# Kernel optimization log

Hardware: AMD Instinct MI355X
Metric: run time of the kernel (lower is better)

## Reference

```python
import jax, jax.numpy as jnp
import numpy as np

B, T, I, H, O = 128, 512, 256, 512, 256


def setup_inputs() -> dict:
    key = jax.random.key(0)
    ks = jax.random.split(key, 20)
    s_i = 1.0 / np.sqrt(I)
    s_h = 1.0 / np.sqrt(H)
    inp = {
        "x": jax.random.normal(ks[0], (B, T, I), dtype=jnp.float32),
        "Wix_w": jax.random.normal(ks[1], (H, I), dtype=jnp.float32) * s_i,
        "Wix_b": jax.random.normal(ks[2], (H,), dtype=jnp.float32) * s_i,
        "Wih_w": jax.random.normal(ks[3], (H, H), dtype=jnp.float32) * s_h,
        "Wih_b": jax.random.normal(ks[4], (H,), dtype=jnp.float32) * s_h,
        "bi": jnp.zeros((H,), dtype=jnp.float32),
        "Wfx_w": jax.random.normal(ks[5], (H, I), dtype=jnp.float32) * s_i,
        "Wfx_b": jax.random.normal(ks[6], (H,), dtype=jnp.float32) * s_i,
        "Wfh_w": jax.random.normal(ks[7], (H, H), dtype=jnp.float32) * s_h,
        "Wfh_b": jax.random.normal(ks[8], (H,), dtype=jnp.float32) * s_h,
        "bf": jnp.zeros((H,), dtype=jnp.float32),
        "Wgx_w": jax.random.normal(ks[9], (H, I), dtype=jnp.float32) * s_i,
        "Wgx_b": jax.random.normal(ks[10], (H,), dtype=jnp.float32) * s_i,
        "Wgh_w": jax.random.normal(ks[11], (H, H), dtype=jnp.float32) * s_h,
        "Wgh_b": jax.random.normal(ks[12], (H,), dtype=jnp.float32) * s_h,
        "bg": jnp.zeros((H,), dtype=jnp.float32),
        "Wox_w": jax.random.normal(ks[13], (H, I), dtype=jnp.float32) * s_i,
        "Wox_b": jax.random.normal(ks[14], (H,), dtype=jnp.float32) * s_i,
        "Woh_w": jax.random.normal(ks[15], (H, H), dtype=jnp.float32) * s_h,
        "Woh_b": jax.random.normal(ks[16], (H,), dtype=jnp.float32) * s_h,
        "bo": jnp.zeros((H,), dtype=jnp.float32),
        "Wph_w": jax.random.normal(ks[17], (O, H), dtype=jnp.float32) * s_h,
        "Wph_b": jax.random.normal(ks[18], (O,), dtype=jnp.float32) * s_h,
        "bp": jnp.zeros((O,), dtype=jnp.float32),
    }
    return inp


def reference(x, Wix_w, Wix_b, Wih_w, Wih_b, bi,
              Wfx_w, Wfx_b, Wfh_w, Wfh_b, bf,
              Wgx_w, Wgx_b, Wgh_w, Wgh_b, bg,
              Wox_w, Wox_b, Woh_w, Woh_b, bo,
              Wph_w, Wph_b, bp):
    batch = x.shape[0]
    h0 = jnp.zeros((batch, Wih_w.shape[0]), dtype=x.dtype)
    c0 = jnp.zeros_like(h0)

    # Precompute all input projections across time in 4 big GEMMs
    # (same math as per-step Linear calls, just batched over t).
    ix = jnp.einsum('bti,hi->bth', x, Wix_w) + Wix_b + bi
    fx = jnp.einsum('bti,hi->bth', x, Wfx_w) + Wfx_b + bf
    gx = jnp.einsum('bti,hi->bth', x, Wgx_w) + Wgx_b + bg
    ox = jnp.einsum('bti,hi->bth', x, Wox_w) + Wox_b + bo

    def step(carry, xt):
        h, c = carry
        ixt, fxt, gxt, oxt = xt
        i = jax.nn.sigmoid(ixt + h @ Wih_w.T + Wih_b)
        f = jax.nn.sigmoid(fxt + h @ Wfh_w.T + Wfh_b)
        g = jnp.tanh(gxt + h @ Wgh_w.T + Wgh_b)
        o = jax.nn.sigmoid(oxt + h @ Woh_w.T + Woh_b)
        c_new = g * i + c * f
        h_new = jnp.tanh(c_new) * o
        p = h_new @ Wph_w.T + Wph_b + bp
        y = jax.nn.softmax(p, axis=1)
        return (h_new, c_new), y

    # scan over time: [T, B, H] layout
    xs = (jnp.swapaxes(ix, 0, 1), jnp.swapaxes(fx, 0, 1),
          jnp.swapaxes(gx, 0, 1), jnp.swapaxes(ox, 0, 1))
    _, ys = jax.lax.scan(step, (h0, c0), xs)
    return jnp.swapaxes(ys, 0, 1)  # [B, T, O]
```

## Files before the change

### kernel.cpp

```cpp
#include <hip/hip_runtime.h>
#include <hip/hip_bf16.h>
#include <math.h>

#define B_  128
#define T_  512
#define I_  256
#define H_  512
#define O_  256
#define NP  2048
#define BT  65536
#define HB  65536

struct PrepArgs {
    const float* Whw[4];
    const float* Wxw[4];
    const float* Wxb[4];
    const float* Whb[4];
    const float* bg[4];
    const float* Wph_w;
    const float* Wph_b;
    const float* bp;
    float* Wt; float* Wg; float* WgT; float* WphT;
    float* xb; float* hb; float* pb;
};

#define PREP_TOTAL (1048576 + 524288 + 524288 + 131072 + 2048 + 2048 + 256)

__global__ __launch_bounds__(256) void k_prep(PrepArgs a) {
    int idx = blockIdx.x * 256 + threadIdx.x;
    if (idx >= PREP_TOTAL) return;
    int q = idx;
    if (q < 1048576) {
        int k = q >> 11, n = q & 2047;
        int g = n & 3, h = n >> 2;
        a.Wt[q] = a.Whw[g][h * H_ + k];
        return;
    }
    q -= 1048576;
    if (q < 524288) {
        int n = q >> 8, i = q & 255;
        int g = n & 3, h = n >> 2;
        a.Wg[q] = a.Wxw[g][h * I_ + i];
        return;
    }
    q -= 524288;
    if (q < 524288) {
        int i = q >> 11, n = q & 2047;
        int g = n & 3, h = n >> 2;
        a.WgT[q] = a.Wxw[g][h * I_ + i];
        return;
    }
    q -= 524288;
    if (q < 131072) {
        int h = q >> 8, o = q & 255;
        a.WphT[q] = a.Wph_w[o * H_ + h];
        return;
    }
    q -= 131072;
    if (q < 2048) {
        int g = q & 3, h = q >> 2;
        a.xb[q] = a.Wxb[g][h] + a.bg[g][h];
        return;
    }
    q -= 2048;
    if (q < 2048) {
        int g = q & 3, h = q >> 2;
        a.hb[q] = a.Whb[g][h];
        return;
    }
    q -= 2048;
    a.pb[q] = a.Wph_b[q] + a.bp[q];
}

__global__ __launch_bounds__(256) void k_transpose(const float* __restrict__ x,
                                                   float* __restrict__ xT2) {
    __shared__ float lds[32][33];
    int tid = threadIdx.x;
    int tx = tid & 31, ty = tid >> 5;
    int j0 = blockIdx.x * 32;
    int i0 = blockIdx.y * 32;
    int t  = j0 >> 7;
    int b0 = j0 & 127;
#pragma unroll
    for (int rr = 0; rr < 4; ++rr) {
        int jj = ty + rr * 8;
        lds[jj][tx] = x[((size_t)(b0 + jj) * T_ + t) * I_ + i0 + tx];
    }
    __syncthreads();
#pragma unroll
    for (int rr = 0; rr < 4; ++rr) {
        int ii = ty + rr * 8;
        xT2[(size_t)(i0 + ii) * BT + j0 + tx] = lds[tx][ii];
    }
}

__global__ __launch_bounds__(256, 1) void k_xgemm(const float* __restrict__ A,
                                                  const float* __restrict__ Bm,
                                                  const float* __restrict__ bias,
                                                  float* __restrict__ C) {
    __shared__ float As[16][128];
    __shared__ float Bs[16][128];
    int tid = threadIdx.x;
    int tx = tid & 15, ty = tid >> 4;
    int m0 = blockIdx.y * 128, j0 = blockIdx.x * 128;
    float acc[8][8];
#pragma unroll
    for (int i = 0; i < 8; ++i)
#pragma unroll
        for (int j = 0; j < 8; ++j) acc[i][j] = 0.f;

    for (int kt = 0; kt < I_; kt += 16) {
#pragma unroll
        for (int pp = 0; pp < 2; ++pp) {
            int p = tid + pp * 256;
            int row = p >> 2, kq = (p & 3) << 2;
            float4 av = *(const float4*)&A[(size_t)(m0 + row) * I_ + kt + kq];
            As[kq + 0][row] = av.x; As[kq + 1][row] = av.y;
            As[kq + 2][row] = av.z; As[kq + 3][row] = av.w;
        }
#pragma unroll
        for (int pp = 0; pp < 2; ++pp) {
            int p = tid + pp * 256;
            int krow = p >> 5, c4 = (p & 31) << 2;
            *(float4*)&Bs[krow][c4] =
                *(const float4*)&Bm[(size_t)(kt + krow) * BT + j0 + c4];
        }
        __syncthreads();
#pragma unroll
        for (int k = 0; k < 16; ++k) {
            float a[8], b[8];
            *(float4*)&a[0] = *(const float4*)&As[k][ty * 4];
            *(float4*)&a[4] = *(const float4*)&As[k][64 + ty * 4];
            *(float4*)&b[0] = *(const float4*)&Bs[k][tx * 4];
            *(float4*)&b[4] = *(const float4*)&Bs[k][64 + tx * 4];
#pragma unroll
            for (int i = 0; i < 8; ++i)
#pragma unroll
                for (int j = 0; j < 8; ++j) acc[i][j] += a[i] * b[j];
        }
        __syncthreads();
    }
#pragma unroll
    for (int i = 0; i < 8; ++i) {
        int mrow = (i < 4) ? (ty * 4 + i) : (64 + ty * 4 + (i - 4));
        int m = m0 + mrow;
        float bv = bias[m];
        float4 v0 = {acc[i][0] + bv, acc[i][1] + bv, acc[i][2] + bv, acc[i][3] + bv};
        float4 v1 = {acc[i][4] + bv, acc[i][5] + bv, acc[i][6] + bv, acc[i][7] + bv};
        *(float4*)&C[(size_t)m * BT + j0 + tx * 4] = v0;
        *(float4*)&C[(size_t)m * BT + j0 + 64 + tx * 4] = v1;
    }
}

__device__ inline float sigm(float v) { return 1.f / (1.f + expf(-v)); }

template <bool USE_XP>
__global__ __launch_bounds__(256, 1) void k_step(const float* __restrict__ Wt,
                                                 const float* __restrict__ WgT,
                                                 const float* __restrict__ xp,
                                                 const float* __restrict__ xT2,
                                                 const float* __restrict__ xb,
                                                 const float* __restrict__ hb,
                                                 float* __restrict__ hist,
                                                 float* __restrict__ cT,
                                                 int t) {
    __shared__ float red[4][16][64];
    int tid = threadIdx.x;
    int wave = tid >> 6, lane = tid & 63;
    int nt = blockIdx.x >> 1, bh = blockIdx.x & 1;
    int n0 = nt * 16, b0 = bh * 64;
    int b = b0 + lane;

    const float* hrow = hist + (size_t)t * HB;
    float acc[16];
#pragma unroll
    for (int j = 0; j < 16; ++j) acc[j] = 0.f;

    {
        int k0 = wave * 128;
        const float* hp = hrow + (size_t)k0 * B_ + b;
        const float* wp = Wt + (size_t)k0 * NP + n0;
        float hv[8];
#pragma unroll
        for (int u = 0; u < 8; ++u) hv[u] = hp[u * B_];
        for (int kb = 0; kb < 128; kb += 8) {
            float hn[8];
            if (kb + 8 < 128) {
                const float* hp2 = hp + (size_t)(kb + 8) * B_;
#pragma unroll
                for (int u = 0; u < 8; ++u) hn[u] = hp2[u * B_];
            }
#pragma unroll
            for (int u = 0; u < 8; ++u) {
                const float* w = wp + (size_t)(kb + u) * NP;
                float h0 = hv[u];
#pragma unroll
                for (int j = 0; j < 4; ++j) {
                    float4 wv = *(const float4*)(w + j * 4);
                    acc[j * 4 + 0] += h0 * wv.x;
                    acc[j * 4 + 1] += h0 * wv.y;
                    acc[j * 4 + 2] += h0 * wv.z;
                    acc[j * 4 + 3] += h0 * wv.w;
                }
            }
#pragma unroll
            for (int u = 0; u < 8; ++u) hv[u] = hn[u];
        }
    }
    if (!USE_XP) {
        int i0 = wave * 64;
        const float* xpp = xT2 + (size_t)i0 * BT + (size_t)t * B_ + b;
        const float* wp  = WgT + (size_t)i0 * NP + n0;
#pragma unroll 4
        for (int ii = 0; ii < 64; ++ii) {
            float xv = xpp[(size_t)ii * BT];
            const float* w = wp + (size_t)ii * NP;
#pragma unroll
            for (int j = 0; j < 4; ++j) {
                float4 wv = *(const float4*)(w + j * 4);
                acc[j * 4 + 0] += xv * wv.x;
                acc[j * 4 + 1] += xv * wv.y;
                acc[j * 4 + 2] += xv * wv.z;
                acc[j * 4 + 3] += xv * wv.w;
            }
        }
    }
#pragma unroll
    for (int j = 0; j < 16; ++j) red[wave][j][lane] = acc[j];
    __syncthreads();

    int b_l = tid & 63, h_i = tid >> 6;
    int n = n0 + h_i * 4;
    int h = nt * 4 + h_i;
    int bb = b0 + b_l;
    float pre[4];
#pragma unroll
    for (int g = 0; g < 4; ++g) {
        int j = h_i * 4 + g;
        pre[g] = red[0][j][b_l] + red[1][j][b_l] + red[2][j][b_l] + red[3][j][b_l];
        pre[g] += hb[n + g];
        if (USE_XP)
            pre[g] += xp[(size_t)(n + g) * BT + (size_t)t * B_ + bb];
        else
            pre[g] += xb[n + g];
    }
    float iv = sigm(pre[0]);
    float fv = sigm(pre[1]);
    float gv = tanhf(pre[2]);
    float ov = sigm(pre[3]);
    float c  = cT[h * B_ + bb];
    float cn = gv * iv + c * fv;
    cT[h * B_ + bb] = cn;
    hist[(size_t)(t + 1) * HB + h * B_ + bb] = tanhf(cn) * ov;
}

__global__ __launch_bounds__(256, 1) void k_outproj(const float* __restrict__ WphT,
                                                    const float* __restrict__ pb,
                                                    const float* __restrict__ hist,
                                                    float* __restrict__ pT) {
    __shared__ float red[4][16][64];
    int tid = threadIdx.x;
    int wave = tid >> 6, lane = tid & 63;
    int t = blockIdx.y;
    int ot = blockIdx.x >> 1, bh = blockIdx.x & 1;
    int o0 = ot * 16, b0 = bh * 64;
    int b = b0 + lane;

    const float* hrow = hist + (size_t)(t + 1) * HB;
    float acc[16];
#pragma unroll
    for (int j = 0; j < 16; ++j) acc[j] = 0.f;

    int k0 = wave * 128;
    const float* hp = hrow + (size_t)k0 * B_ + b;
    const float* wp = WphT + (size_t)k0 * O_ + o0;
    float hv[8];
#pragma unroll
    for (int u = 0; u < 8; ++u) hv[u] = hp[u * B_];
    for (int kb = 0; kb < 128; kb += 8) {
        float hn[8];
        if (kb + 8 < 128) {
            const float* hp2 = hp + (size_t)(kb + 8) * B_;
#pragma unroll
            for (int u = 0; u < 8; ++u) hn[u] = hp2[u * B_];
        }
#pragma unroll
        for (int u = 0; u < 8; ++u) {
            const float* w = wp + (size_t)(kb + u) * O_;
            float h0 = hv[u];
#pragma unroll
            for (int j = 0; j < 4; ++j) {
                float4 wv = *(const float4*)(w + j * 4);
                acc[j * 4 + 0] += h0 * wv.x;
                acc[j * 4 + 1] += h0 * wv.y;
                acc[j * 4 + 2] += h0 * wv.z;
                acc[j * 4 + 3] += h0 * wv.w;
            }
        }
#pragma unroll
        for (int u = 0; u < 8; ++u) hv[u] = hn[u];
    }
#pragma unroll
    for (int j = 0; j < 16; ++j) red[wave][j][lane] = acc[j];
    __syncthreads();

    int b_l = tid & 63, oi = tid >> 6;
    int bb = b0 + b_l;
#pragma unroll
    for (int g = 0; g < 4; ++g) {
        int j = oi * 4 + g;
        int o = o0 + j;
        float v = red[0][j][b_l] + red[1][j][b_l] + red[2][j][b_l] + red[3][j][b_l] + pb[o];
        pT[(size_t)t * (O_ * B_) + (size_t)o * B_ + bb] = v;
    }
}

__global__ __launch_bounds__(256, 1) void k_softmax(const float* __restrict__ pT,
                                                    float* __restrict__ out) {
    __shared__ float sm[32][257];
    __shared__ float rmax[32][8];
    __shared__ float rsum[32][8];
    int tid = threadIdx.x;
    int t = blockIdx.x >> 2, bq = blockIdx.x & 3;
    int b0 = bq * 32;
    const float* src = pT + (size_t)t * (O_ * B_);

#pragma unroll 4
    for (int it = 0; it < 32; ++it) {
        int idx = it * 256 + tid;
        int o = idx >> 5, b_l = idx & 31;
        sm[b_l][o] = src[(size_t)o * B_ + b0 + b_l];
    }
    __syncthreads();

    int b_l = tid >> 3, oc = tid & 7;
    float m = -3.4e38f;
#pragma unroll 4
    for (int oo = 0; oo < 32; ++oo) m = fmaxf(m, sm[b_l][oc * 32 + oo]);
    rmax[b_l][oc] = m;
    __syncthreads();
    float mm = rmax[b_l][0];
#pragma unroll
    for (int c = 1; c < 8; ++c) mm = fmaxf(mm, rmax[b_l][c]);

    float s = 0.f;
#pragma unroll 4
    for (int oo = 0; oo < 32; ++oo) s += expf(sm[b_l][oc * 32 + oo] - mm);
    rsum[b_l][oc] = s;
    __syncthreads();
    float st = 0.f;
#pragma unroll
    for (int c = 0; c < 8; ++c) st += rsum[b_l][c];
    float inv = 1.f / st;

    int bb = b0 + b_l;
    float* dst = out + ((size_t)bb * T_ + t) * O_ + oc * 32;
#pragma unroll 4
    for (int oo = 0; oo < 32; ++oo)
        dst[oo] = expf(sm[b_l][oc * 32 + oo] - mm) * inv;
}

extern "C" void kernel_launch(void* const* d_in, const int* in_sizes, int n_in,
                              void* d_out, int out_size, void* d_ws, size_t ws_size,
                              hipStream_t stream) {
    const float* x = (const float*)d_in[0];

    float* ws = (float*)d_ws;
    size_t off = 0;
    auto alloc = [&](size_t n) { float* p = ws + off; off += n; return p; };

    float* hist = alloc((size_t)513 * HB);
    float* cT   = alloc(HB);
    float* Wt   = alloc((size_t)512 * NP);
    float* Wg   = alloc((size_t)NP * I_);
    float* WgT  = alloc((size_t)I_ * NP);
    float* WphT = alloc((size_t)H_ * O_);
    float* xb   = alloc(NP);
    float* hb   = alloc(NP);
    float* pb   = alloc(O_);
    float* xT2  = alloc((size_t)I_ * BT);
    size_t baseBytes = off * sizeof(float);
    size_t xpBytes   = (size_t)NP * BT * sizeof(float);

    bool useXp = (ws_size >= baseBytes + xpBytes);
    float* xp = ws + off;
    float* pT = xT2;

    if (ws_size < baseBytes) return;

    hipMemsetAsync(hist, 0, HB * sizeof(float), stream);
    hipMemsetAsync(cT, 0, HB * sizeof(float), stream);

    PrepArgs pa;
    for (int g = 0; g < 4; ++g) {
        pa.Wxw[g] = (const float*)d_in[1 + 5 * g];
        pa.Wxb[g] = (const float*)d_in[2 + 5 * g];
        pa.Whw[g] = (const float*)d_in[3 + 5 * g];
        pa.Whb[g] = (const float*)d_in[4 + 5 * g];
        pa.bg[g]  = (const float*)d_in[5 + 5 * g];
    }
    pa.Wph_w = (const float*)d_in[21];
    pa.Wph_b = (const float*)d_in[22];
    pa.bp    = (const float*)d_in[23];
    pa.Wt = Wt; pa.Wg = Wg; pa.WgT = WgT; pa.WphT = WphT;
    pa.xb = xb; pa.hb = hb; pa.pb = pb;

    k_prep<<<(PREP_TOTAL + 255) / 256, 256, 0, stream>>>(pa);
    k_transpose<<<dim3(BT / 32, I_ / 32), 256, 0, stream>>>(x, xT2);

    if (useXp)
        k_xgemm<<<dim3(BT / 128, NP / 128), 256, 0, stream>>>(Wg, xT2, xb, xp);

    for (int t = 0; t < T_; ++t) {
        if (useXp)
            k_step<true><<<256, 256, 0, stream>>>(Wt, WgT, xp, xT2, xb, hb, hist, cT, t);
        else
            k_step<false><<<256, 256, 0, stream>>>(Wt, WgT, xp, xT2, xb, hb, hist, cT, t);
    }

    k_outproj<<<dim3(32, T_), 256, 0, stream>>>(WphT, pb, hist, pT);
    k_softmax<<<T_ * 4, 256, 0, stream>>>(pT, (float*)d_out);
}
```

Measured before the change: 17.03 ms.

## Replace per-timestep launches with persistent weight-stationary scan kernel and grid barriers

Replaces the 512 per-step kernel launches and the precomputed input-projection GEMM with a single persistent kernel. Each block keeps its slice of the recurrent and input weights in registers and handles 8 batch rows. Blocks synchronise each step through per-group atomic counters in global memory, and the input projection is computed inside the loop. The output projection now writes logits straight into the output, softmax runs in place, and the h history layout changes to batch-major. This removes launch overhead and the xp GEMM traffic, but it depends on all 256 blocks being co-resident, since the spin barrier would otherwise deadlock, and the bounded spin loop could silently break.

Result: slower. 29.47 ms (+73.1%).

```diff
diff --git a/kernel.cpp b/kernel.cpp
--- a/kernel.cpp
+++ b/kernel.cpp
@@ -10,6 +10,7 @@
 #define NP  2048
 #define BT  65536
 #define HB  65536
+
 
 struct PrepArgs {
     const float* Whw[4];
@@ -20,11 +21,11 @@
     const float* Wph_w;
     const float* Wph_b;
     const float* bp;
-    float* Wt; float* Wg; float* WgT; float* WphT;
-    float* xb; float* hb; float* pb;
+    float* Wt; float* WgT; float* WphT;
+    float* cb; float* pb;
 };
 
-#define PREP_TOTAL (1048576 + 524288 + 524288 + 131072 + 2048 + 2048 + 256)
+#define PREP_TOTAL (1048576 + 524288 + 131072 + 2048 + 256)
 
 __global__ __launch_bounds__(256) void k_prep(PrepArgs a) {
     int idx = blockIdx.x * 256 + threadIdx.x;
@@ -38,13 +39,6 @@
     }
     q -= 1048576;
     if (q < 524288) {
-        int n = q >> 8, i = q & 255;
-        int g = n & 3, h = n >> 2;
-        a.Wg[q] = a.Wxw[g][h * I_ + i];
-        return;
-    }
-    q -= 524288;
-    if (q < 524288) {
         int i = q >> 11, n = q & 2047;
         int g = n & 3, h = n >> 2;
         a.WgT[q] = a.Wxw[g][h * I_ + i];
@@ -59,71 +53,211 @@
     q -= 131072;
     if (q < 2048) {
         int g = q & 3, h = q >> 2;
-        a.xb[q] = a.Wxb[g][h] + a.bg[g][h];
-        return;
-    }
-    q -= 2048;
-    if (q < 2048) {
-        int g = q & 3, h = q >> 2;
-        a.hb[q] = a.Whb[g][h];
+        a.cb[q] = a.Wxb[g][h] + a.bg[g][h] + a.Whb[g][h];
         return;
     }
     q -= 2048;
     a.pb[q] = a.Wph_b[q] + a.bp[q];
 }
 
-__global__ __launch_bounds__(256) void k_transpose(const float* __restrict__ x,
-                                                   float* __restrict__ xT2) {
+__global__ __launch_bounds__(256) void k_xT3(const float* __restrict__ x,
+                                             float* __restrict__ xT3) {
     __shared__ float lds[32][33];
     int tid = threadIdx.x;
     int tx = tid & 31, ty = tid >> 5;
-    int j0 = blockIdx.x * 32;
+    int b0 = blockIdx.x * 32;
     int i0 = blockIdx.y * 32;
-    int t  = j0 >> 7;
-    int b0 = j0 & 127;
+    int t  = blockIdx.z;
 #pragma unroll
     for (int rr = 0; rr < 4; ++rr) {
-        int jj = ty + rr * 8;
-        lds[jj][tx] = x[((size_t)(b0 + jj) * T_ + t) * I_ + i0 + tx];
+        int bb = ty + rr * 8;
+        lds[bb][tx] = x[((size_t)(b0 + bb) * T_ + t) * I_ + i0 + tx];
     }
     __syncthreads();
 #pragma unroll
     for (int rr = 0; rr < 4; ++rr) {
         int ii = ty + rr * 8;
-        xT2[(size_t)(i0 + ii) * BT + j0 + tx] = lds[tx][ii];
-    }
-}
-
-__global__ __launch_bounds__(256, 1) void k_xgemm(const float* __restrict__ A,
-                                                  const float* __restrict__ Bm,
-                                                  const float* __restrict__ bias,
-                                                  float* __restrict__ C) {
+        xT3[((size_t)t * I_ + i0 + ii) * B_ + b0 + tx] = lds[tx][ii];
+    }
+}
+
+__device__ inline float sigm(float v) { return 1.f / (1.f + expf(-v)); }
+
+__global__ __launch_bounds__(512, 2) void k_scanp(const float* __restrict__ Wt,
+                                                  const float* __restrict__ WgT,
+                                                  const float* __restrict__ xT3,
+                                                  const float* __restrict__ cb,
+                                                  float* __restrict__ hist,
+                                                  int* __restrict__ bar) {
+    __shared__ float x_lds[8 * 260];
+    __shared__ float h_lds[8 * 516];
+    __shared__ float red[8 * 128 * 12];
+
+    int tid = threadIdx.x;
+    int wave = tid >> 6, lane = tid & 63;
+    int jb  = blockIdx.x & 15;
+    int grp = blockIdx.x >> 4;
+    int n0  = jb * 128;
+    int kc  = wave * 64;
+    int ic  = wave * 32;
+    int bg0 = grp * 8;
+
+    float w0[64], w1[64];
+#pragma unroll
+    for (int k = 0; k < 64; ++k) {
+        w0[k] = Wt[(size_t)(kc + k) * NP + n0 + lane];
+        w1[k] = Wt[(size_t)(kc + k) * NP + n0 + 64 + lane];
+    }
+    float xw0[32], xw1[32];
+#pragma unroll
+    for (int i = 0; i < 32; ++i) {
+        xw0[i] = WgT[(size_t)(ic + i) * NP + n0 + lane];
+        xw1[i] = WgT[(size_t)(ic + i) * NP + n0 + 64 + lane];
+    }
+
+    int h_i = tid >> 3, b_l = tid & 7;
+    float cbv[4] = {0, 0, 0, 0};
+    float c_reg = 0.f;
+    if (tid < 256) {
+#pragma unroll
+        for (int g = 0; g < 4; ++g) cbv[g] = cb[n0 + h_i * 4 + g];
+    }
+
+    for (int t = 0; t < T_; ++t) {
+        {
+            int i = tid >> 1, q = (tid & 1) * 4;
+            float4 xv = *(const float4*)&xT3[((size_t)t * I_ + i) * B_ + bg0 + q];
+            x_lds[(q + 0) * 260 + i] = xv.x;
+            x_lds[(q + 1) * 260 + i] = xv.y;
+            x_lds[(q + 2) * 260 + i] = xv.z;
+            x_lds[(q + 3) * 260 + i] = xv.w;
+        }
+        __syncthreads();
+
+        float acc0[8], acc1[8];
+#pragma unroll
+        for (int b = 0; b < 8; ++b) { acc0[b] = 0.f; acc1[b] = 0.f; }
+#pragma unroll
+        for (int i4 = 0; i4 < 8; ++i4) {
+#pragma unroll
+            for (int b = 0; b < 8; ++b) {
+                float4 xv = *(const float4*)&x_lds[b * 260 + ic + i4 * 4];
+                acc0[b] = fmaf(xw0[i4 * 4 + 0], xv.x, acc0[b]);
+                acc0[b] = fmaf(xw0[i4 * 4 + 1], xv.y, acc0[b]);
+                acc0[b] = fmaf(xw0[i4 * 4 + 2], xv.z, acc0[b]);
+                acc0[b] = fmaf(xw0[i4 * 4 + 3], xv.w, acc0[b]);
+                acc1[b] = fmaf(xw1[i4 * 4 + 0], xv.x, acc1[b]);
+                acc1[b] = fmaf(xw1[i4 * 4 + 1], xv.y, acc1[b]);
+                acc1[b] = fmaf(xw1[i4 * 4 + 2], xv.z, acc1[b]);
+                acc1[b] = fmaf(xw1[i4 * 4 + 3], xv.w, acc1[b]);
+            }
+        }
+
+        if (t > 0 && tid == 0) {
+            const int* c = bar + (t - 1) * 16 + grp;
+            int spins = 0;
+            while (__hip_atomic_load(c, __ATOMIC_RELAXED,
+                                     __HIP_MEMORY_SCOPE_AGENT) < 16) {
+                __builtin_amdgcn_s_sleep(1);
+                if (++spins > 10000000) break;
+            }
+        }
+        __syncthreads();
+        __builtin_amdgcn_fence(__ATOMIC_ACQUIRE, "agent");
+
+        {
+            int k8 = lane * 8;
+            const float* src = hist + (size_t)t * HB + (size_t)(bg0 + wave) * 512 + k8;
+            float* dst = h_lds + wave * 516 + k8;
+            *(float4*)(dst + 0) = *(const float4*)(src + 0);
+            *(float4*)(dst + 4) = *(const float4*)(src + 4);
+        }
+        __syncthreads();
+
+#pragma unroll
+        for (int k4 = 0; k4 < 16; ++k4) {
+#pragma unroll
+            for (int b = 0; b < 8; ++b) {
+                float4 hv = *(const float4*)&h_lds[b * 516 + kc + k4 * 4];
+                acc0[b] = fmaf(w0[k4 * 4 + 0], hv.x, acc0[b]);
+                acc0[b] = fmaf(w0[k4 * 4 + 1], hv.y, acc0[b]);
+                acc0[b] = fmaf(w0[k4 * 4 + 2], hv.z, acc0[b]);
+                acc0[b] = fmaf(w0[k4 * 4 + 3], hv.w, acc0[b]);
+                acc1[b] = fmaf(w1[k4 * 4 + 0], hv.x, acc1[b]);
+                acc1[b] = fmaf(w1[k4 * 4 + 1], hv.y, acc1[b]);
+                acc1[b] = fmaf(w1[k4 * 4 + 2], hv.z, acc1[b]);
+                acc1[b] = fmaf(w1[k4 * 4 + 3], hv.w, acc1[b]);
+            }
+        }
+
+        {
+            float* r0 = &red[(wave * 128 + lane) * 12];
+            float* r1 = &red[(wave * 128 + 64 + lane) * 12];
+            *(float4*)(r0 + 0) = *(float4*)&acc0[0];
+            *(float4*)(r0 + 4) = *(float4*)&acc0[4];
+            *(float4*)(r1 + 0) = *(float4*)&acc1[0];
+            *(float4*)(r1 + 4) = *(float4*)&acc1[4];
+        }
+        __syncthreads();
+
+        if (tid < 256) {
+            float pre[4];
+#pragma unroll
+            for (int g = 0; g < 4; ++g) {
+                int col = h_i * 4 + g;
+                float s = 0.f;
+#pragma unroll
+                for (int w = 0; w < 8; ++w) s += red[(w * 128 + col) * 12 + b_l];
+                pre[g] = s + cbv[g];
+            }
+            float iv = sigm(pre[0]);
+            float fv = sigm(pre[1]);
+            float gv = tanhf(pre[2]);
+            float ov = sigm(pre[3]);
+            c_reg = gv * iv + c_reg * fv;
+            hist[(size_t)(t + 1) * HB + (size_t)(bg0 + b_l) * 512 + (jb * 32 + h_i)] =
+                tanhf(c_reg) * ov;
+        }
+        __syncthreads();
+        if (tid == 0)
+            __hip_atomic_fetch_add(bar + t * 16 + grp, 1, __ATOMIC_RELEASE,
+                                   __HIP_MEMORY_SCOPE_AGENT);
+    }
+}
+
+__global__ __launch_bounds__(256, 1) void k_outproj(const float* __restrict__ hist,
+                                                    const float* __restrict__ WphT,
+                                                    const float* __restrict__ pb,
+                                                    float* __restrict__ out) {
     __shared__ float As[16][128];
     __shared__ float Bs[16][128];
     int tid = threadIdx.x;
     int tx = tid & 15, ty = tid >> 4;
-    int m0 = blockIdx.y * 128, j0 = blockIdx.x * 128;
+    int t = blockIdx.y;
+    int o0 = blockIdx.x * 128;
+    const float* A = hist + (size_t)(t + 1) * HB;
     float acc[8][8];
 #pragma unroll
     for (int i = 0; i < 8; ++i)
 #pragma unroll
-        for (int j = 0; j < 8; ++j) acc[i][j] = 0.f;
-
-    for (int kt = 0; kt < I_; kt += 16) {
+        for (int jj = 0; jj < 8; ++jj) acc[i][jj] = 0.f;
+
+    for (int kt = 0; kt < H_; kt += 16) {
 #pragma unroll
         for (int pp = 0; pp < 2; ++pp) {
             int p = tid + pp * 256;
             int row = p >> 2, kq = (p & 3) << 2;
-            float4 av = *(const float4*)&A[(size_t)(m0 + row) * I_ + kt + kq];
+            float4 av = *(const float4*)&A[(size_t)row * H_ + kt + kq];
             As[kq + 0][row] = av.x; As[kq + 1][row] = av.y;
             As[kq + 2][row] = av.z; As[kq + 3][row] = av.w;
         }
-#pragma unroll
-        for (int pp = 0; pp < 2; ++pp) {
-            int p = tid + pp * 256;
-            int krow = p >> 5, c4 = (p & 31) << 2;
+        {
+            int krow = tid >> 5, c4 = (tid & 31) << 2;
             *(float4*)&Bs[krow][c4] =
-                *(const float4*)&Bm[(size_t)(kt + krow) * BT + j0 + c4];
+                *(const float4*)&WphT[(size_t)(kt + krow) * O_ + o0 + c4];
+            int krow2 = krow + 8;
+            *(float4*)&Bs[krow2][c4] =
+                *(const float4*)&WphT[(size_t)(kt + krow2) * O_ + o0 + c4];
         }
         __syncthreads();
 #pragma unroll
@@ -136,228 +270,62 @@
 #pragma unroll
             for (int i = 0; i < 8; ++i)
 #pragma unroll
-                for (int j = 0; j < 8; ++j) acc[i][j] += a[i] * b[j];
-        }
-        __syncthreads();
-    }
+                for (int jj = 0; jj < 8; ++jj) acc[i][jj] += a[i] * b[jj];
+        }
+        __syncthreads();
+    }
+    float4 bv0 = *(const float4*)&pb[o0 + tx * 4];
+    float4 bv1 = *(const float4*)&pb[o0 + 64 + tx * 4];
 #pragma unroll
     for (int i = 0; i < 8; ++i) {
         int mrow = (i < 4) ? (ty * 4 + i) : (64 + ty * 4 + (i - 4));
-        int m = m0 + mrow;
-        float bv = bias[m];
-        float4 v0 = {acc[i][0] + bv, acc[i][1] + bv, acc[i][2] + bv, acc[i][3] + bv};
-        float4 v1 = {acc[i][4] + bv, acc[i][5] + bv, acc[i][6] + bv, acc[i][7] + bv};
-        *(float4*)&C[(size_t)m * BT + j0 + tx * 4] = v0;
-        *(float4*)&C[(size_t)m * BT + j0 + 64 + tx * 4] = v1;
-    }
-}
-
-__device__ inline float sigm(float v) { return 1.f / (1.f + expf(-v)); }
-
-template <bool USE_XP>
-__global__ __launch_bounds__(256, 1) void k_step(const float* __restrict__ Wt,
-                                                 const float* __restrict__ WgT,
-                                                 const float* __restrict__ xp,
-                                                 const float* __restrict__ xT2,
-                                                 const float* __restrict__ xb,
-                                                 const float* __restrict__ hb,
-                                                 float* __restrict__ hist,
-                                                 float* __restrict__ cT,
-                                                 int t) {
-    __shared__ float red[4][16][64];
-    int tid = threadIdx.x;
-    int wave = tid >> 6, lane = tid & 63;
-    int nt = blockIdx.x >> 1, bh = blockIdx.x & 1;
-    int n0 = nt * 16, b0 = bh * 64;
-    int b = b0 + lane;
-
-    const float* hrow = hist + (size_t)t * HB;
-    float acc[16];
-#pragma unroll
-    for (int j = 0; j < 16; ++j) acc[j] = 0.f;
-
-    {
-        int k0 = wave * 128;
-        const float* hp = hrow + (size_t)k0 * B_ + b;
-        const float* wp = Wt + (size_t)k0 * NP + n0;
-        float hv[8];
-#pragma unroll
-        for (int u = 0; u < 8; ++u) hv[u] = hp[u * B_];
-        for (int kb = 0; kb < 128; kb += 8) {
-            float hn[8];
-            if (kb + 8 < 128) {
-                const float* hp2 = hp + (size_t)(kb + 8) * B_;
-#pragma unroll
-                for (int u = 0; u < 8; ++u) hn[u] = hp2[u * B_];
-            }
-#pragma unroll
-            for (int u = 0; u < 8; ++u) {
-                const float* w = wp + (size_t)(kb + u) * NP;
-                float h0 = hv[u];
-#pragma unroll
-                for (int j = 0; j < 4; ++j) {
-                    float4 wv = *(const float4*)(w + j * 4);
-                    acc[j * 4 + 0] += h0 * wv.x;
-                    acc[j * 4 + 1] += h0 * wv.y;
-                    acc[j * 4 + 2] += h0 * wv.z;
-                    acc[j * 4 + 3] += h0 * wv.w;
-                }
-            }
-#pragma unroll
-            for (int u = 0; u < 8; ++u) hv[u] = hn[u];
-        }
-    }
-    if (!USE_XP) {
-        int i0 = wave * 64;
-        const float* xpp = xT2 + (size_t)i0 * BT + (size_t)t * B_ + b;
-        const float* wp  = WgT + (size_t)i0 * NP + n0;
-#pragma unroll 4
-        for (int ii = 0; ii < 64; ++ii) {
-            float xv = xpp[(size_t)ii * BT];
-            const float* w = wp + (size_t)ii * NP;
-#pragma unroll
-            for (int j = 0; j < 4; ++j) {
-                float4 wv = *(const float4*)(w + j * 4);
-                acc[j * 4 + 0] += xv * wv.x;
-                acc[j * 4 + 1] += xv * wv.y;
-                acc[j * 4 + 2] += xv * wv.z;
-                acc[j * 4 + 3] += xv * wv.w;
-            }
-        }
-    }
-#pragma unroll
-    for (int j = 0; j < 16; ++j) red[wave][j][lane] = acc[j];
-    __syncthreads();
-
-    int b_l = tid & 63, h_i = tid >> 6;
-    int n = n0 + h_i * 4;
-    int h = nt * 4 + h_i;
-    int bb = b0 + b_l;
-    float pre[4];
-#pragma unroll
-    for (int g = 0; g < 4; ++g) {
-        int j = h_i * 4 + g;
-        pre[g] = red[0][j][b_l] + red[1][j][b_l] + red[2][j][b_l] + red[3][j][b_l];
-        pre[g] += hb[n + g];
-        if (USE_XP)
-            pre[g] += xp[(size_t)(n + g) * BT + (size_t)t * B_ + bb];
-        else
-            pre[g] += xb[n + g];
-    }
-    float iv = sigm(pre[0]);
-    float fv = sigm(pre[1]);
-    float gv = tanhf(pre[2]);
-    float ov = sigm(pre[3]);
-    float c  = cT[h * B_ + bb];
-    float cn = gv * iv + c * fv;
-    cT[h * B_ + bb] = cn;
-    hist[(size_t)(t + 1) * HB + h * B_ + bb] = tanhf(cn) * ov;
-}
-
-__global__ __launch_bounds__(256, 1) void k_outproj(const float* __restrict__ WphT,
-                                                    const float* __restrict__ pb,
-                                                    const float* __restrict__ hist,
-                                                    float* __restrict__ pT) {
-    __shared__ float red[4][16][64];
-    int tid = threadIdx.x;
-    int wave = tid >> 6, lane = tid & 63;
-    int t = blockIdx.y;
-    int ot = blockIdx.x >> 1, bh = blockIdx.x & 1;
-    int o0 = ot * 16, b0 = bh * 64;
-    int b = b0 + lane;
-
-    const float* hrow = hist + (size_t)(t + 1) * HB;
-    float acc[16];
-#pragma unroll
-    for (int j = 0; j < 16; ++j) acc[j] = 0.f;
-
-    int k0 = wave * 128;
-    const float* hp = hrow + (size_t)k0 * B_ + b;
-    const float* wp = WphT + (size_t)k0 * O_ + o0;
-    float hv[8];
-#pragma unroll
-    for (int u = 0; u < 8; ++u) hv[u] = hp[u * B_];
-    for (int kb = 0; kb < 128; kb += 8) {
-        float hn[8];
-        if (kb + 8 < 128) {
-            const float* hp2 = hp + (size_t)(kb + 8) * B_;
-#pragma unroll
-            for (int u = 0; u < 8; ++u) hn[u] = hp2[u * B_];
-        }
-#pragma unroll
-        for (int u = 0; u < 8; ++u) {
-            const float* w = wp + (size_t)(kb + u) * O_;
-            float h0 = hv[u];
-#pragma unroll
-            for (int j = 0; j < 4; ++j) {
-                float4 wv = *(const float4*)(w + j * 4);
-                acc[j * 4 + 0] += h0 * wv.x;
-                acc[j * 4 + 1] += h0 * wv.y;
-                acc[j * 4 + 2] += h0 * wv.z;
-                acc[j * 4 + 3] += h0 * wv.w;
-            }
-        }
-#pragma unroll
-        for (int u = 0; u < 8; ++u) hv[u] = hn[u];
-    }
-#pragma unroll
-    for (int j = 0; j < 16; ++j) red[wave][j][lane] = acc[j];
-    __syncthreads();
-
-    int b_l = tid & 63, oi = tid >> 6;
-    int bb = b0 + b_l;
-#pragma unroll
-    for (int g = 0; g < 4; ++g) {
-        int j = oi * 4 + g;
-        int o = o0 + j;
-        float v = red[0][j][b_l] + red[1][j][b_l] + red[2][j][b_l] + red[3][j][b_l] + pb[o];
-        pT[(size_t)t * (O_ * B_) + (size_t)o * B_ + bb] = v;
-    }
-}
-
-__global__ __launch_bounds__(256, 1) void k_softmax(const float* __restrict__ pT,
-                                                    float* __restrict__ out) {
-    __shared__ float sm[32][257];
+        float4 v0 = {acc[i][0] + bv0.x, acc[i][1] + bv0.y,
+                     acc[i][2] + bv0.z, acc[i][3] + bv0.w};
+        float4 v1 = {acc[i][4] + bv1.x, acc[i][5] + bv1.y,
+                     acc[i][6] + bv1.z, acc[i][7] + bv1.w};
+        float* dst = out + ((size_t)mrow * T_ + t) * O_ + o0;
+        *(float4*)(dst + tx * 4) = v0;
+        *(float4*)(dst + 64 + tx * 4) = v1;
+    }
+}
+
+__global__ __launch_bounds__(256, 1) void k_softmax(float* __restrict__ out) {
+    __shared__ float sm[32][260];
     __shared__ float rmax[32][8];
     __shared__ float rsum[32][8];
     int tid = threadIdx.x;
     int t = blockIdx.x >> 2, bq = blockIdx.x & 3;
     int b0 = bq * 32;
-    const float* src = pT + (size_t)t * (O_ * B_);
-
-#pragma unroll 4
-    for (int it = 0; it < 32; ++it) {
-        int idx = it * 256 + tid;
-        int o = idx >> 5, b_l = idx & 31;
-        sm[b_l][o] = src[(size_t)o * B_ + b0 + b_l];
-    }
+    int r = tid >> 3, oc = tid & 7;
+    float* base = out + ((size_t)(b0 + r) * T_ + t) * O_ + oc * 32;
+
+#pragma unroll
+    for (int q = 0; q < 8; ++q)
+        *(float4*)&sm[r][oc * 32 + q * 4] = *(const float4*)(base + q * 4);
     __syncthreads();
 
-    int b_l = tid >> 3, oc = tid & 7;
     float m = -3.4e38f;
-#pragma unroll 4
-    for (int oo = 0; oo < 32; ++oo) m = fmaxf(m, sm[b_l][oc * 32 + oo]);
-    rmax[b_l][oc] = m;
+#pragma unroll
+    for (int oo = 0; oo < 32; ++oo) m = fmaxf(m, sm[r][oc * 32 + oo]);
+    rmax[r][oc] = m;
     __syncthreads();
-    float mm = rmax[b_l][0];
-#pragma unroll
-    for (int c = 1; c < 8; ++c) mm = fmaxf(mm, rmax[b_l][c]);
+    float mm = rmax[r][0];
+#pragma unroll
+    for (int c = 1; c < 8; ++c) mm = fmaxf(mm, rmax[r][c]);
 
     float s = 0.f;
-#pragma unroll 4
-    for (int oo = 0; oo < 32; ++oo) s += expf(sm[b_l][oc * 32 + oo] - mm);
-    rsum[b_l][oc] = s;
+#pragma unroll
+    for (int oo = 0; oo < 32; ++oo) s += expf(sm[r][oc * 32 + oo] - mm);
+    rsum[r][oc] = s;
     __syncthreads();
     float st = 0.f;
 #pragma unroll
-    for (int c = 0; c < 8; ++c) st += rsum[b_l][c];
+    for (int c = 0; c < 8; ++c) st += rsum[r][c];
     float inv = 1.f / st;
 
-    int bb = b0 + b_l;
-    float* dst = out + ((size_t)bb * T_ + t) * O_ + oc * 32;
-#pragma unroll 4
+#pragma unroll
     for (int oo = 0; oo < 32; ++oo)
-        dst[oo] = expf(sm[b_l][oc * 32 + oo] - mm) * inv;
+        base[oo] = expf(sm[r][oc * 32 + oo] - mm) * inv;
 }
 
 extern "C" void kernel_launch(void* const* d_in, const int* in_sizes, int n_in,
@@ -370,26 +338,18 @@
     auto alloc = [&](size_t n) { float* p = ws + off; off += n; return p; };
 
     float* hist = alloc((size_t)513 * HB);
-    float* cT   = alloc(HB);
     float* Wt   = alloc((size_t)512 * NP);
-    float* Wg   = alloc((size_t)NP * I_);
     float* WgT  = alloc((size_t)I_ * NP);
     float* WphT = alloc((size_t)H_ * O_);
-    float* xb   = alloc(NP);
-    float* hb   = alloc(NP);
+    float* cb   = alloc(NP);
     float* pb   = alloc(O_);
-    float* xT2  = alloc((size_t)I_ * BT);
-    size_t baseBytes = off * sizeof(float);
-    size_t xpBytes   = (size_t)NP * BT * sizeof(float);
-
-    bool useXp = (ws_size >= baseBytes + xpBytes);
-    float* xp = ws + off;
-    float* pT = xT2;
-
-    if (ws_size < baseBytes) return;
+    int*   bar  = (int*)alloc((size_t)512 * 16);
+    float* xT3  = alloc((size_t)T_ * I_ * B_);
+
+    if (ws_size < off * sizeof(float)) return;
 
     hipMemsetAsync(hist, 0, HB * sizeof(float), stream);
-    hipMemsetAsync(cT, 0, HB * sizeof(float), stream);
+    hipMemsetAsync(bar, 0, (size_t)512 * 16 * sizeof(int), stream);
 
     PrepArgs pa;
     for (int g = 0; g < 4; ++g) {
@@ -402,22 +362,14 @@
     pa.Wph_w = (const float*)d_in[21];
     pa.Wph_b = (const float*)d_in[22];
     pa.bp    = (const float*)d_in[23];
-    pa.Wt = Wt; pa.Wg = Wg; pa.WgT = WgT; pa.WphT = WphT;
-    pa.xb = xb; pa.hb = hb; pa.pb = pb;
+    pa.Wt = Wt; pa.WgT = WgT; pa.WphT = WphT;
+    pa.cb = cb; pa.pb = pb;
 
     k_prep<<<(PREP_TOTAL + 255) / 256, 256, 0, stream>>>(pa);
-    k_transpose<<<dim3(BT / 32, I_ / 32), 256, 0, stream>>>(x, xT2);
-
-    if (useXp)
-        k_xgemm<<<dim3(BT / 128, NP / 128), 256, 0, stream>>>(Wg, xT2, xb, xp);
-
-    for (int t = 0; t < T_; ++t) {
-        if (useXp)
-            k_step<true><<<256, 256, 0, stream>>>(Wt, WgT, xp, xT2, xb, hb, hist, cT, t);
-        else
-            k_step<false><<<256, 256, 0, stream>>>(Wt, WgT, xp, xT2, xb, hb, hist, cT, t);
-    }
-
-    k_outproj<<<dim3(32, T_), 256, 0, stream>>>(WphT, pb, hist, pT);
-    k_softmax<<<T_ * 4, 256, 0, stream>>>(pT, (float*)d_out);
-}
+    k_xT3<<<dim3(4, 8, 512), 256, 0, stream>>>(x, xT3);
+
+    k_scanp<<<256, 512, 0, stream>>>(Wt, WgT, xT3, cb, hist, bar);
+
+    k_outproj<<<dim3(2, T_), 256, 0, stream>>>(hist, WphT, pb, (float*)d_out);
+    k_softmax<<<T_ * 4, 256, 0, stream>>>((float*)d_out);
+}
```
